# Kernel optimization log

Measured on AMD Instinct MI355X. Metric: run time of the kernel, lower is better.

The kernel has to match this reference:

```python
import jax, jax.numpy as jnp
import numpy as np


def _offdiag_cols(B):
    # cols[i, k] = k-th column index != i, ascending (matches masked_select on ~eye)
    r = jnp.arange(B - 1)[None, :]
    i = jnp.arange(B)[:, None]
    return jnp.where(r < i, r, r + 1)  # [B, B-1]


def _process_case(lan_s, vis, B):
    # lan_s: [B, D], vis: [B, V, D]
    lan_adj = lan_s @ lan_s.T                               # [B, B]
    # sim[b, a, v] = lan_s[b] . vis[a, v]  (torch 'avd,bqd->baqv' with q=1)
    sim = jnp.einsum('avd,bd->bav', vis, lan_s)             # [B, B, V]
    vals, idxs = jax.lax.top_k(sim, 2)                      # [B, B, 2]
    ar = jnp.arange(B)
    diag_idx = idxs[ar, ar, 0]                              # best region per matched pair
    selected = vis[ar, diag_idx]                            # [B, D]
    img_adj = selected @ selected.T                         # [B, B]
    # Slogits [B,B,1,1] -> max over trailing dims == plain matmul
    logits = selected @ lan_s.T                             # [B, B]

    max0 = vals[..., 0]                                     # [B, B]
    max1 = vals[..., 1]                                     # [B, B]
    cols = _offdiag_cols(B)
    max1_off = jnp.take_along_axis(max1, cols, axis=1)      # [B, B-1]
    new_logits = jnp.concatenate([max0, max1_off], axis=1)  # [B, 2B-1]
    # CrossEntropyLoss(mean) with target = arange(B)
    ce = -jnp.mean(jax.nn.log_softmax(new_logits, axis=1)[ar, ar])

    # Regularization pair loss on row-softmaxed max0; neg idx for sample i = all j != i,
    # duplicated (t2i and i2t are identical here) -> duplication cancels in the mean.
    score = jax.nn.softmax(max0, axis=1)                    # [B, B]
    d = jnp.diag(score)                                     # s_ii
    offmask = (1.0 - jnp.eye(B, dtype=score.dtype))
    denom = jnp.asarray(B * (B - 1), score.dtype)
    # t1[i,j] = |(s_ii - s_ji) - (s_jj - s_ij)|, t2[i,j] = |(s_ii - s_ij) - (s_jj - s_ji)|
    t1 = jnp.abs(d[:, None] - score.T - d[None, :] + score)
    t2 = jnp.abs(d[:, None] - score - d[None, :] + score.T)
    m1 = jnp.sum(t1 * offmask) / denom
    m2 = jnp.sum(t2 * offmask) / denom
    pairloss = jax.nn.relu(m1) + jax.nn.relu(m2)            # (L1 - margin).clamp(0), margin=0

    # L1 between adjacency softmax and logits softmax
    loss_fns = jnp.mean(jnp.abs(
        jax.nn.softmax((img_adj + lan_adj) * 0.5, axis=1) -
        jax.nn.softmax(logits, axis=1)))

    alpha = jnp.asarray(0.1, score.dtype)
    beta = jnp.asarray(0.1, score.dtype)
    return ce + alpha * loss_fns + beta * pairloss


def reference(vis_fs, lan_fs):
    B = vis_fs.shape[0]
    losses = [_process_case(lan_fs[:, i, :], vis_fs, B) for i in range(3)]
    return (losses[0] + losses[1] + losses[2]) / 3.0


def setup_inputs() -> dict:
    key = jax.random.key(0)
    k1, k2 = jax.random.split(key)
    B, V, D = 128, 784, 512
    # scale ~0.05 so dot products of D=512-dim embeddings stay in a sane softmax range
    vis_fs = jax.random.normal(k1, (B, V, D), dtype=jnp.float32) * 0.05
    lan_fs = jax.random.normal(k2, (B, 3, D), dtype=jnp.float32) * 0.05
    return {"vis_fs": vis_fs, "lan_fs": lan_fs}
```

## Files before the change

kernel.cpp:

```cpp
#include <hip/hip_runtime.h>
#include <math.h>

#define B_   128
#define V_   784
#define D_   512
#define M_   384
#define NCH  7

typedef __attribute__((ext_vector_type(8))) short short8;
typedef __attribute__((ext_vector_type(4))) float f32x4;
typedef unsigned int u32t;

__device__ __forceinline__ ushort f2bf(float x) {
  uint u = __float_as_uint(x);
  u += 0x7fff + ((u >> 16) & 1);
  return (ushort)(u >> 16);
}
__device__ __forceinline__ float bf2f(ushort h) {
  return __uint_as_float((uint)h << 16);
}

__device__ __forceinline__ void stage16(const void* g, void* l) {
  __builtin_amdgcn_global_load_lds(
      (const __attribute__((address_space(1))) u32t*)g,
      (__attribute__((address_space(3))) u32t*)(uintptr_t)l, 16, 0, 0);
}

__global__ __launch_bounds__(256)
void prep_lan(const float* __restrict__ lan, ushort* __restrict__ lanbf,
              float* __restrict__ acc) {
  const int c = blockIdx.x >> 4, s = blockIdx.x & 15, t = threadIdx.x;
  if (blockIdx.x == 0 && t < 12) acc[t] = 0.f;
  #pragma unroll
  for (int it = 0; it < 2; ++it) {
    const int u = t + it * 256;
    const int m16 = u >> 6, lane = u & 63;
    const int row = m16 * 16 + (lane & 15);
    const int k = s * 32 + (lane >> 4) * 8;
    const float* src = lan + (size_t)(row * 3 + c) * D_ + k;
    const float4 v0 = *(const float4*)src;
    const float4 v1 = *(const float4*)(src + 4);
    union { ushort s[8]; uint4 q; } H, L;
    const float f[8] = {v0.x, v0.y, v0.z, v0.w, v1.x, v1.y, v1.z, v1.w};
    #pragma unroll
    for (int e = 0; e < 8; ++e) {
      const ushort h = f2bf(f[e]);
      H.s[e] = h; L.s[e] = f2bf(f[e] - bf2f(h));
    }
    const size_t base = ((size_t)(c * 16 + s) * 2) * 8 * 512;
    *(uint4*)&lanbf[base + (size_t)m16 * 512 + lane * 8] = H.q;
    *(uint4*)&lanbf[base + 4096 + (size_t)m16 * 512 + lane * 8] = L.q;
  }
}

__global__ __launch_bounds__(512, 2)
void gemm_top2(const float* __restrict__ vis, const ushort* __restrict__ lanbf,
               float* __restrict__ pv1, float* __restrict__ pv2,
               int* __restrict__ pi1) {
  __shared__ __align__(16) char Lds[131072];

  const int id = blockIdx.x;
  const int a = id / NCH;
  const int nch = id - NCH * a;
  const int t = threadIdx.x;
  const int lane = t & 63, wid = t >> 6;
  const int tx = lane & 15, qq = lane >> 4;
  const int wr = wid >> 1, wc = wid & 1;
  const int v0 = nch * 128;
  const char* visA = (const char*)vis + (size_t)a * V_ * D_ * 4;

  const char* gb[8];
  int gstep[8], ldso[8];
  #pragma unroll
  for (int gq = 0; gq < 8; ++gq) {
    const int I = wid * 8 + gq;
    ldso[gq] = I * 1024;
    if (I < 48) {
      const int c = I >> 4, sub = I & 15;
      gb[gq] = (const char*)lanbf + (size_t)c * 262144 + sub * 1024 + lane * 16;
      gstep[gq] = 16384;
    } else {
      const int v16 = (I - 48) >> 1, hb = (I - 48) & 1;
      const int vp = (lane >> 1) & 15;
      const int q2 = hb * 2 + (lane >> 5);
      const int f4 = lane & 1;
      int v = v0 + v16 * 16 + vp;
      if (v > V_ - 1) v = V_ - 1;
      gb[gq] = visA + (size_t)v * 2048 + q2 * 32 + f4 * 16;
      gstep[gq] = 128;
    }
  }

  f32x4 acc[3][2][4];
  const f32x4 zz = {0.f, 0.f, 0.f, 0.f};
  #pragma unroll
  for (int c = 0; c < 3; ++c)
    #pragma unroll
    for (int m = 0; m < 2; ++m)
      #pragma unroll
      for (int n = 0; n < 4; ++n) acc[c][m][n] = zz;

  #pragma unroll
  for (int gq = 0; gq < 8; ++gq) stage16(gb[gq], Lds + ldso[gq]);
  asm volatile("s_waitcnt vmcnt(0)" ::: "memory");
  __builtin_amdgcn_s_barrier();
  asm volatile("" ::: "memory");

  for (int s = 0; s < 16; ++s) {
    const int buf = s & 1;
    char* Lb = Lds + buf * 65536;
    if (s < 15) {
      char* Ln = Lds + (buf ^ 1) * 65536;
      #pragma unroll
      for (int gq = 0; gq < 8; ++gq)
        stage16(gb[gq] + (size_t)(s + 1) * gstep[gq], Ln + ldso[gq]);
    }
    short8 bh[4], bl[4];
    #pragma unroll
    for (int n = 0; n < 4; ++n) {
      const char* bp = Lb + 49152 + (wc * 4 + n) * 2048 + lane * 32;
      const float4 x = *(const float4*)bp;
      const float4 y = *(const float4*)(bp + 16);
      union { ushort s[8]; short8 v; } H, L;
      const float f[8] = {x.x, x.y, x.z, x.w, y.x, y.y, y.z, y.w};
      #pragma unroll
      for (int e = 0; e < 8; ++e) {
        const ushort h = f2bf(f[e]);
        H.s[e] = h; L.s[e] = f2bf(f[e] - bf2f(h));
      }
      bh[n] = H.v; bl[n] = L.v;
    }
    #pragma unroll
    for (int c = 0; c < 3; ++c) {
      short8 ah[2], al[2];
      #pragma unroll
      for (int m = 0; m < 2; ++m) {
        const int sub = wr * 2 + m;
        ah[m] = *(const short8*)(Lb + (c * 16 + sub) * 1024 + lane * 16);
        al[m] = *(const short8*)(Lb + (c * 16 + 8 + sub) * 1024 + lane * 16);
      }
      #pragma unroll
      for (int m = 0; m < 2; ++m)
        #pragma unroll
        for (int n = 0; n < 4; ++n) {
          acc[c][m][n] = __builtin_amdgcn_mfma_f32_16x16x32_bf16(
              ah[m], bh[n], acc[c][m][n], 0, 0, 0);
          acc[c][m][n] = __builtin_amdgcn_mfma_f32_16x16x32_bf16(
              ah[m], bl[n], acc[c][m][n], 0, 0, 0);
          acc[c][m][n] = __builtin_amdgcn_mfma_f32_16x16x32_bf16(
              al[m], bh[n], acc[c][m][n], 0, 0, 0);
        }
    }
    if (s < 15) asm volatile("s_waitcnt vmcnt(0)" ::: "memory");
    __builtin_amdgcn_s_barrier();
    asm volatile("" ::: "memory");
  }

  float* p1b = (float*)Lds;
  float* p2b = p1b + 256;
  int*   i1b = (int*)(p2b + 256);
  #pragma unroll
  for (int c = 0; c < 3; ++c) {
    #pragma unroll
    for (int m = 0; m < 2; ++m)
      #pragma unroll
      for (int r = 0; r < 4; ++r) {
        float v1 = -INFINITY, v2 = -INFINITY;
        int i1 = 0x7fffffff;
        #pragma unroll
        for (int n = 0; n < 4; ++n) {
          const int vv = v0 + wc * 64 + n * 16 + tx;
          const float x = acc[c][m][n][r];
          if (vv < V_) {
            if (x > v1) { v2 = v1; v1 = x; i1 = vv; }
            else if (x > v2) { v2 = x; }
          }
        }
        #pragma unroll
        for (int off = 8; off >= 1; off >>= 1) {
          const float ov1 = __shfl_xor(v1, off, 16);
          const float ov2 = __shfl_xor(v2, off, 16);
          const int   oi1 = __shfl_xor(i1, off, 16);
          if (ov1 > v1 || (ov1 == v1 && oi1 < i1)) {
            v2 = fmaxf(v1, ov2); v1 = ov1; i1 = oi1;
          } else {
            v2 = fmaxf(v2, ov1);
          }
        }
        if (tx == 0) {
          const int grow = wr * 32 + m * 16 + qq * 4 + r;
          p1b[wc * 128 + grow] = v1;
          p2b[wc * 128 + grow] = v2;
          i1b[wc * 128 + grow] = i1;
        }
      }
    __syncthreads();
    if (t < 128) {
      float v1 = p1b[t], v2 = p2b[t];
      int i1 = i1b[t];
      const float ov1 = p1b[128 + t], ov2 = p2b[128 + t];
      const int oi1 = i1b[128 + t];
      if (ov1 > v1) { v2 = fmaxf(v1, ov2); v1 = ov1; i1 = oi1; }
      else          { v2 = fmaxf(v2, ov1); }
      const size_t o = ((size_t)a * NCH + nch) * M_ + c * B_ + t;
      pv1[o] = v1; pv2[o] = v2; pi1[o] = i1;
    }
    __syncthreads();
  }
}

__global__ void reduce_top2(const float* __restrict__ pv1,
                            const float* __restrict__ pv2,
                            const int* __restrict__ pi1,
                            float* __restrict__ max0, float* __restrict__ max1,
                            int* __restrict__ didx) {
  const int idx = blockIdx.x * 256 + threadIdx.x;
  if (idx >= M_ * B_) return;
  const int m = idx >> 7, a = idx & 127;
  float v1 = -INFINITY, v2 = -INFINITY;
  int i1 = 0x7fffffff;
  #pragma unroll
  for (int nc = 0; nc < NCH; nc++) {
    const size_t o = ((size_t)a * NCH + nc) * M_ + m;
    const float ov1 = pv1[o], ov2 = pv2[o];
    const int oi1 = pi1[o];
    if (ov1 > v1 || (ov1 == v1 && oi1 < i1)) {
      v2 = fmaxf(v1, ov2); v1 = ov1; i1 = oi1;
    } else {
      v2 = fmaxf(v2, ov1);
    }
  }
  max0[idx] = v1;
  max1[idx] = v2;
  const int b = m & 127, cc = m >> 7;
  if (b == a) didx[(cc << 7) + b] = i1;
}

__global__ void gather_sel(const float* __restrict__ vis,
                           const int* __restrict__ didx,
                           float* __restrict__ sel) {
  const int cb = blockIdx.x;
  const int b = cb & 127;
  const int v = didx[cb];
  const float4* src = (const float4*)(vis + ((size_t)b * V_ + v) * D_);
  float4* dst = (float4*)(sel + (size_t)cb * D_);
  dst[threadIdx.x] = src[threadIdx.x];
}

__device__ __forceinline__ float wsum64(float v) {
  #pragma unroll
  for (int m = 32; m >= 1; m >>= 1) v += __shfl_xor(v, m);
  return v;
}
__device__ __forceinline__ float wmax64(float v) {
  #pragma unroll
  for (int m = 32; m >= 1; m >>= 1) v = fmaxf(v, __shfl_xor(v, m));
  return v;
}
__device__ __forceinline__ float halfsum(float v, float* sb, int rr, int t) {
  v = wsum64(v);
  __syncthreads();
  if ((t & 63) == 0) sb[t >> 6] = v;
  __syncthreads();
  return sb[rr * 2] + sb[rr * 2 + 1];
}
__device__ __forceinline__ float halfmax(float v, float* sb, int rr, int t) {
  v = wmax64(v);
  __syncthreads();
  if ((t & 63) == 0) sb[t >> 6] = v;
  __syncthreads();
  return fmaxf(sb[rr * 2], sb[rr * 2 + 1]);
}

__global__ __launch_bounds__(256)
void adj_losses(const float* __restrict__ lan, const float* __restrict__ sel,
                const float* __restrict__ max0, const float* __restrict__ max1,
                float* __restrict__ score, float* __restrict__ acc) {
  __shared__ float sb[4];
  __shared__ float sdiag[2];
  const int c = blockIdx.y;
  const int t = threadIdx.x;
  const int rr = t >> 7, j = t & 127;
  const int i = blockIdx.x * 2 + rr;

  const float4* xl = (const float4*)(lan + (size_t)(i * 3 + c) * D_);
  const float4* xs = (const float4*)(sel + ((size_t)c * B_ + i) * D_);
  const float4* yl = (const float4*)(lan + (size_t)(j * 3 + c) * D_);
  const float4* ys = (const float4*)(sel + ((size_t)c * B_ + j) * D_);
  float sll = 0.f, sss = 0.f, ssl = 0.f;
  #pragma unroll 4
  for (int k = 0; k < D_ / 4; ++k) {
    const float4 A = xl[k], Bv = yl[k], C = xs[k], Dv = ys[k];
    sll += A.x * Bv.x + A.y * Bv.y + A.z * Bv.z + A.w * Bv.w;
    sss += C.x * Dv.x + C.y * Dv.y + C.z * Dv.z + C.w * Dv.w;
    ssl += C.x * Bv.x + C.y * Bv.y + C.z * Bv.z + C.w * Bv.w;
  }
  const float u = 0.5f * (sll + sss);
  const float g = ssl;

  const size_t row = ((size_t)c * B_ + i) * B_;
  const float m0 = max0[row + j];
  const float m1 = (j == i) ? -INFINITY : max1[row + j];
  if (j == i) sdiag[rr] = m0;

  const float rmax = halfmax(fmaxf(m0, m1), sb, rr, t);
  const float se =
      halfsum(expf(m0 - rmax) + ((j == i) ? 0.f : expf(m1 - rmax)), sb, rr, t);
  if (j == 0) atomicAdd(&acc[c], logf(se) + rmax - sdiag[rr]);

  const float smax = halfmax(m0, sb, rr, t);
  const float e0 = expf(m0 - smax);
  const float ssum = halfsum(e0, sb, rr, t);
  score[row + j] = e0 / ssum;

  const float umax = halfmax(u, sb, rr, t);
  const float eu = expf(u - umax);
  const float usum = halfsum(eu, sb, rr, t);
  const float gmax = halfmax(g, sb, rr, t);
  const float eg = expf(g - gmax);
  const float gsum = halfsum(eg, sb, rr, t);
  const float dsum = halfsum(fabsf(eu / usum - eg / gsum), sb, rr, t);
  if (j == 0) atomicAdd(&acc[3 + c], dsum);
}

__global__ __launch_bounds__(1024)
void pair_finalize(const float* __restrict__ score, const float* __restrict__ acc,
                   float* __restrict__ out) {
  __shared__ float diag[M_];
  __shared__ float sb[16];
  const int t = threadIdx.x;
  if (t < M_) diag[t] = score[(size_t)t * 128 + (t & 127)];
  __syncthreads();

  float gtot = 0.f;
  #pragma unroll
  for (int c = 0; c < 3; ++c) {
    float t1 = 0.f, t2 = 0.f;
    const float* S = score + (size_t)c * (B_ * B_);
    const float* Dg = diag + c * B_;
    #pragma unroll
    for (int it = 0; it < 16; ++it) {
      const int ij = it * 1024 + t;
      const int i = ij >> 7, j = ij & 127;
      if (i != j) {
        const float sij = S[i * B_ + j], sji = S[j * B_ + i];
        const float dii = Dg[i], djj = Dg[j];
        t1 += fabsf(dii - sji - djj + sij);
        t2 += fabsf(dii - sij - djj + sji);
      }
    }
    t1 = wsum64(t1);
    t2 = wsum64(t2);
    __syncthreads();
    if ((t & 63) == 0) sb[t >> 6] = t1;
    __syncthreads();
    float r1 = 0.f, r2 = 0.f;
    if (t == 0) {
      #pragma unroll
      for (int w = 0; w < 16; ++w) r1 += sb[w];
    }
    __syncthreads();
    if ((t & 63) == 0) sb[t >> 6] = t2;
    __syncthreads();
    if (t == 0) {
      #pragma unroll
      for (int w = 0; w < 16; ++w) r2 += sb[w];
      const float den = (float)(B_ * (B_ - 1));
      const float ce = acc[c] / (float)B_;
      const float fns = acc[3 + c] / (float)(B_ * B_);
      gtot += ce + 0.1f * fns +
              0.1f * (fmaxf(r1 / den, 0.f) + fmaxf(r2 / den, 0.f));
    }
    __syncthreads();
  }
  if (t == 0) out[0] = gtot / 3.f;
}

extern "C" void kernel_launch(void* const* d_in, const int* in_sizes, int n_in,
                              void* d_out, int out_size, void* d_ws, size_t ws_size,
                              hipStream_t stream) {
  const float* vis = (const float*)d_in[0];
  const float* lan = (const float*)d_in[1];
  float* out = (float*)d_out;

  float* w = (float*)d_ws;
  float* pv1 = w;
  float* pv2 = pv1 + (size_t)M_ * B_ * NCH;
  int*   pi1 = (int*)(pv2 + (size_t)M_ * B_ * NCH);
  float* max0 = (float*)(pi1 + (size_t)M_ * B_ * NCH);
  float* max1 = max0 + 3 * B_ * B_;
  int*   didx = (int*)(max1 + 3 * B_ * B_);
  float* sel  = (float*)(didx + 3 * B_);
  float* score = sel + (size_t)3 * B_ * D_;
  float* acc   = score + 3 * B_ * B_;
  ushort* lanbf = (ushort*)(acc + 16);

  prep_lan<<<dim3(48), dim3(256), 0, stream>>>(lan, lanbf, acc);
  gemm_top2<<<dim3(B_ * NCH), dim3(512), 0, stream>>>(vis, lanbf, pv1, pv2, pi1);
  reduce_top2<<<dim3((M_ * B_ + 255) / 256), dim3(256), 0, stream>>>(
      pv1, pv2, pi1, max0, max1, didx);
  gather_sel<<<dim3(3 * B_), dim3(128), 0, stream>>>(vis, didx, sel);
  adj_losses<<<dim3(B_ / 2, 3), dim3(256), 0, stream>>>(
      lan, sel, max0, max1, score, acc);
  pair_finalize<<<dim3(1), dim3(1024), 0, stream>>>(score, acc, out);
}
```

Before: 532.1 us.

## Convert vis tiles to bf16 split once per block into LDS, restructure reductions

The main GEMM kernel now loads the fp32 vis tile with register loads, converts it once into hi/lo bf16 pairs and writes them into a double-buffered LDS region. Before, every wave redundantly converted fp32 data read from LDS. This cuts LDS footprint and repeated conversion ALU work, but the global vis loads now go through registers rather than direct-to-LDS loads. Separately, reduce_top2 is remapped so each block handles one a with coalesced partial reads, and adj_losses uses one row per block with the row vectors cached in LDS and a two-thread split of the K loop.

```diff
diff --git a/kernel.cpp b/kernel.cpp
--- a/kernel.cpp
+++ b/kernel.cpp
@@ -47,10 +47,23 @@
       const ushort h = f2bf(f[e]);
       H.s[e] = h; L.s[e] = f2bf(f[e] - bf2f(h));
     }
-    const size_t base = ((size_t)(c * 16 + s) * 2) * 8 * 512;
+    const size_t base = ((size_t)(c * 16 + s) * 2) * 4096;
     *(uint4*)&lanbf[base + (size_t)m16 * 512 + lane * 8] = H.q;
     *(uint4*)&lanbf[base + 4096 + (size_t)m16 * 512 + lane * 8] = L.q;
   }
+}
+
+__device__ __forceinline__ void cvt_write(char* base, int t,
+                                          float4 b0, float4 b1) {
+  union { ushort s[8]; uint4 q; } H, L;
+  const float f[8] = {b0.x, b0.y, b0.z, b0.w, b1.x, b1.y, b1.z, b1.w};
+  #pragma unroll
+  for (int e = 0; e < 8; ++e) {
+    const ushort h = f2bf(f[e]);
+    H.s[e] = h; L.s[e] = f2bf(f[e] - bf2f(h));
+  }
+  *(uint4*)(base + t * 16) = H.q;
+  *(uint4*)(base + 8192 + t * 16) = L.q;
 }
 
 __global__ __launch_bounds__(512, 2)
@@ -67,29 +80,18 @@
   const int tx = lane & 15, qq = lane >> 4;
   const int wr = wid >> 1, wc = wid & 1;
   const int v0 = nch * 128;
-  const char* visA = (const char*)vis + (size_t)a * V_ * D_ * 4;
-
-  const char* gb[8];
-  int gstep[8], ldso[8];
-  #pragma unroll
-  for (int gq = 0; gq < 8; ++gq) {
-    const int I = wid * 8 + gq;
-    ldso[gq] = I * 1024;
-    if (I < 48) {
-      const int c = I >> 4, sub = I & 15;
-      gb[gq] = (const char*)lanbf + (size_t)c * 262144 + sub * 1024 + lane * 16;
-      gstep[gq] = 16384;
-    } else {
-      const int v16 = (I - 48) >> 1, hb = (I - 48) & 1;
-      const int vp = (lane >> 1) & 15;
-      const int q2 = hb * 2 + (lane >> 5);
-      const int f4 = lane & 1;
-      int v = v0 + v16 * 16 + vp;
-      if (v > V_ - 1) v = V_ - 1;
-      gb[gq] = visA + (size_t)v * 2048 + q2 * 32 + f4 * 16;
-      gstep[gq] = 128;
-    }
-  }
+
+  const char* asrc[6];
+  #pragma unroll
+  for (int q = 0; q < 6; ++q) {
+    const int j = wid * 6 + q;
+    const int c = j >> 4, h = (j >> 3) & 1, m16 = j & 7;
+    asrc[q] = (const char*)lanbf + (size_t)c * 262144 + h * 8192 + m16 * 1024 +
+              lane * 16;
+  }
+  int vrow = v0 + (t & 127);
+  if (vrow > V_ - 1) vrow = V_ - 1;
+  const float* bsrc = vis + (size_t)a * (V_ * D_) + (size_t)vrow * D_ + (t >> 7) * 8;
 
   f32x4 acc[3][2][4];
   const f32x4 zz = {0.f, 0.f, 0.f, 0.f};
@@ -101,43 +103,42 @@
       for (int n = 0; n < 4; ++n) acc[c][m][n] = zz;
 
   #pragma unroll
-  for (int gq = 0; gq < 8; ++gq) stage16(gb[gq], Lds + ldso[gq]);
-  asm volatile("s_waitcnt vmcnt(0)" ::: "memory");
-  __builtin_amdgcn_s_barrier();
-  asm volatile("" ::: "memory");
+  for (int q = 0; q < 6; ++q)
+    stage16(asrc[q], Lds + (wid * 6 + q) * 1024);
+  {
+    const float4 b0 = *(const float4*)bsrc;
+    const float4 b1 = *(const float4*)(bsrc + 4);
+    cvt_write(Lds + 98304, t, b0, b1);
+  }
+  __syncthreads();
 
   for (int s = 0; s < 16; ++s) {
-    const int buf = s & 1;
-    char* Lb = Lds + buf * 65536;
+    const int p = s & 1;
+    const char* Ap = Lds + p * 49152;
+    const char* Bp = Lds + 98304 + p * 16384;
+    float4 b0, b1;
     if (s < 15) {
-      char* Ln = Lds + (buf ^ 1) * 65536;
-      #pragma unroll
-      for (int gq = 0; gq < 8; ++gq)
-        stage16(gb[gq] + (size_t)(s + 1) * gstep[gq], Ln + ldso[gq]);
+      char* An = Lds + (p ^ 1) * 49152;
+      #pragma unroll
+      for (int q = 0; q < 6; ++q)
+        stage16(asrc[q] + (size_t)(s + 1) * 16384, An + (wid * 6 + q) * 1024);
+      b0 = *(const float4*)(bsrc + (s + 1) * 32);
+      b1 = *(const float4*)(bsrc + (s + 1) * 32 + 4);
     }
     short8 bh[4], bl[4];
     #pragma unroll
     for (int n = 0; n < 4; ++n) {
-      const char* bp = Lb + 49152 + (wc * 4 + n) * 2048 + lane * 32;
-      const float4 x = *(const float4*)bp;
-      const float4 y = *(const float4*)(bp + 16);
-      union { ushort s[8]; short8 v; } H, L;
-      const float f[8] = {x.x, x.y, x.z, x.w, y.x, y.y, y.z, y.w};
-      #pragma unroll
-      for (int e = 0; e < 8; ++e) {
-        const ushort h = f2bf(f[e]);
-        H.s[e] = h; L.s[e] = f2bf(f[e] - bf2f(h));
-      }
-      bh[n] = H.v; bl[n] = L.v;
+      const int ch = qq * 128 + (wc * 4 + n) * 16 + tx;
+      bh[n] = *(const short8*)(Bp + ch * 16);
+      bl[n] = *(const short8*)(Bp + 8192 + ch * 16);
     }
     #pragma unroll
     for (int c = 0; c < 3; ++c) {
       short8 ah[2], al[2];
       #pragma unroll
       for (int m = 0; m < 2; ++m) {
-        const int sub = wr * 2 + m;
-        ah[m] = *(const short8*)(Lb + (c * 16 + sub) * 1024 + lane * 16);
-        al[m] = *(const short8*)(Lb + (c * 16 + 8 + sub) * 1024 + lane * 16);
+        ah[m] = *(const short8*)(Ap + (c * 16 + wr * 2 + m) * 1024 + lane * 16);
+        al[m] = *(const short8*)(Ap + (c * 16 + 8 + wr * 2 + m) * 1024 + lane * 16);
       }
       #pragma unroll
       for (int m = 0; m < 2; ++m)
@@ -151,9 +152,9 @@
               al[m], bh[n], acc[c][m][n], 0, 0, 0);
         }
     }
-    if (s < 15) asm volatile("s_waitcnt vmcnt(0)" ::: "memory");
-    __builtin_amdgcn_s_barrier();
-    asm volatile("" ::: "memory");
+    if (s < 15)
+      cvt_write(Lds + 98304 + (p ^ 1) * 16384, t, b0, b1);
+    __syncthreads();
   }
 
   float* p1b = (float*)Lds;
@@ -209,14 +210,13 @@
   }
 }
 
-__global__ void reduce_top2(const float* __restrict__ pv1,
-                            const float* __restrict__ pv2,
-                            const int* __restrict__ pi1,
-                            float* __restrict__ max0, float* __restrict__ max1,
-                            int* __restrict__ didx) {
-  const int idx = blockIdx.x * 256 + threadIdx.x;
-  if (idx >= M_ * B_) return;
-  const int m = idx >> 7, a = idx & 127;
+__global__ __launch_bounds__(384)
+void reduce_top2(const float* __restrict__ pv1,
+                 const float* __restrict__ pv2,
+                 const int* __restrict__ pi1,
+                 float* __restrict__ max0, float* __restrict__ max1,
+                 int* __restrict__ didx) {
+  const int a = blockIdx.x, m = threadIdx.x;
   float v1 = -INFINITY, v2 = -INFINITY;
   int i1 = 0x7fffffff;
   #pragma unroll
@@ -230,10 +230,10 @@
       v2 = fmaxf(v2, ov1);
     }
   }
-  max0[idx] = v1;
-  max1[idx] = v2;
+  max0[(size_t)m * B_ + a] = v1;
+  max1[(size_t)m * B_ + a] = v2;
   const int b = m & 127, cc = m >> 7;
-  if (b == a) didx[(cc << 7) + b] = i1;
+  if (b == a) didx[cc * B_ + b] = i1;
 }
 
 __global__ void gather_sel(const float* __restrict__ vis,
@@ -257,70 +257,76 @@
   for (int m = 32; m >= 1; m >>= 1) v = fmaxf(v, __shfl_xor(v, m));
   return v;
 }
-__device__ __forceinline__ float halfsum(float v, float* sb, int rr, int t) {
+__device__ __forceinline__ float bsum4(float v, float* sb, int t) {
   v = wsum64(v);
   __syncthreads();
   if ((t & 63) == 0) sb[t >> 6] = v;
   __syncthreads();
-  return sb[rr * 2] + sb[rr * 2 + 1];
-}
-__device__ __forceinline__ float halfmax(float v, float* sb, int rr, int t) {
+  return sb[0] + sb[1] + sb[2] + sb[3];
+}
+__device__ __forceinline__ float bmax4(float v, float* sb, int t) {
   v = wmax64(v);
   __syncthreads();
   if ((t & 63) == 0) sb[t >> 6] = v;
   __syncthreads();
-  return fmaxf(sb[rr * 2], sb[rr * 2 + 1]);
+  return fmaxf(fmaxf(sb[0], sb[1]), fmaxf(sb[2], sb[3]));
 }
 
 __global__ __launch_bounds__(256)
 void adj_losses(const float* __restrict__ lan, const float* __restrict__ sel,
                 const float* __restrict__ max0, const float* __restrict__ max1,
                 float* __restrict__ score, float* __restrict__ acc) {
+  __shared__ float4 xls[128], xss[128];
   __shared__ float sb[4];
-  __shared__ float sdiag[2];
-  const int c = blockIdx.y;
+  __shared__ float sdiag;
+  const int c = blockIdx.y, i = blockIdx.x;
   const int t = threadIdx.x;
-  const int rr = t >> 7, j = t & 127;
-  const int i = blockIdx.x * 2 + rr;
-
-  const float4* xl = (const float4*)(lan + (size_t)(i * 3 + c) * D_);
-  const float4* xs = (const float4*)(sel + ((size_t)c * B_ + i) * D_);
-  const float4* yl = (const float4*)(lan + (size_t)(j * 3 + c) * D_);
-  const float4* ys = (const float4*)(sel + ((size_t)c * B_ + j) * D_);
+  const int j = t >> 1, h = t & 1;
+
+  if (t < 128) xls[t] = ((const float4*)(lan + (size_t)(i * 3 + c) * D_))[t];
+  else xss[t - 128] = ((const float4*)(sel + ((size_t)c * B_ + i) * D_))[t - 128];
+  __syncthreads();
+
+  const float4* yl = (const float4*)(lan + (size_t)(j * 3 + c) * D_) + h * 64;
+  const float4* ys = (const float4*)(sel + ((size_t)c * B_ + j) * D_) + h * 64;
   float sll = 0.f, sss = 0.f, ssl = 0.f;
   #pragma unroll 4
-  for (int k = 0; k < D_ / 4; ++k) {
-    const float4 A = xl[k], Bv = yl[k], C = xs[k], Dv = ys[k];
+  for (int k = 0; k < 64; ++k) {
+    const float4 A = xls[h * 64 + k], C = xss[h * 64 + k];
+    const float4 Bv = yl[k], Dv = ys[k];
     sll += A.x * Bv.x + A.y * Bv.y + A.z * Bv.z + A.w * Bv.w;
     sss += C.x * Dv.x + C.y * Dv.y + C.z * Dv.z + C.w * Dv.w;
     ssl += C.x * Bv.x + C.y * Bv.y + C.z * Bv.z + C.w * Bv.w;
   }
+  sll += __shfl_xor(sll, 1);
+  sss += __shfl_xor(sss, 1);
+  ssl += __shfl_xor(ssl, 1);
   const float u = 0.5f * (sll + sss);
   const float g = ssl;
 
   const size_t row = ((size_t)c * B_ + i) * B_;
   const float m0 = max0[row + j];
   const float m1 = (j == i) ? -INFINITY : max1[row + j];
-  if (j == i) sdiag[rr] = m0;
-
-  const float rmax = halfmax(fmaxf(m0, m1), sb, rr, t);
-  const float se =
-      halfsum(expf(m0 - rmax) + ((j == i) ? 0.f : expf(m1 - rmax)), sb, rr, t);
-  if (j == 0) atomicAdd(&acc[c], logf(se) + rmax - sdiag[rr]);
-
-  const float smax = halfmax(m0, sb, rr, t);
+  if (j == i && h == 0) sdiag = m0;
+
+  const float rmax = bmax4(fmaxf(m0, m1), sb, t);
+  const float se = 0.5f *
+      bsum4(expf(m0 - rmax) + ((j == i) ? 0.f : expf(m1 - rmax)), sb, t);
+  if (t == 0) atomicAdd(&acc[c], logf(se) + rmax - sdiag);
+
+  const float smax = bmax4(m0, sb, t);
   const float e0 = expf(m0 - smax);
-  const float ssum = halfsum(e0, sb, rr, t);
+  const float ssum = 0.5f * bsum4(e0, sb, t);
   score[row + j] = e0 / ssum;
 
-  const float umax = halfmax(u, sb, rr, t);
+  const float umax = bmax4(u, sb, t);
   const float eu = expf(u - umax);
-  const float usum = halfsum(eu, sb, rr, t);
-  const float gmax = halfmax(g, sb, rr, t);
+  const float usum = 0.5f * bsum4(eu, sb, t);
+  const float gmax = bmax4(g, sb, t);
   const float eg = expf(g - gmax);
-  const float gsum = halfsum(eg, sb, rr, t);
-  const float dsum = halfsum(fabsf(eu / usum - eg / gsum), sb, rr, t);
-  if (j == 0) atomicAdd(&acc[3 + c], dsum);
+  const float gsum = 0.5f * bsum4(eg, sb, t);
+  const float dsum = 0.5f * bsum4(fabsf(eu / usum - eg / gsum), sb, t);
+  if (t == 0) atomicAdd(&acc[3 + c], dsum);
 }
 
 __global__ __launch_bounds__(1024)
@@ -397,10 +403,10 @@
 
   prep_lan<<<dim3(48), dim3(256), 0, stream>>>(lan, lanbf, acc);
   gemm_top2<<<dim3(B_ * NCH), dim3(512), 0, stream>>>(vis, lanbf, pv1, pv2, pi1);
-  reduce_top2<<<dim3((M_ * B_ + 255) / 256), dim3(256), 0, stream>>>(
+  reduce_top2<<<dim3(B_), dim3(384), 0, stream>>>(
       pv1, pv2, pi1, max0, max1, didx);
   gather_sel<<<dim3(3 * B_), dim3(128), 0, stream>>>(vis, didx, sel);
-  adj_losses<<<dim3(B_ / 2, 3), dim3(256), 0, stream>>>(
+  adj_losses<<<dim3(B_, 3), dim3(256), 0, stream>>>(
       lan, sel, max0, max1, score, acc);
   pair_finalize<<<dim3(1), dim3(1024), 0, stream>>>(score, acc, out);
 }
```

Result: faster. 481.6 us (-9.5%).
